# Performance work log

Hardware: AMD Instinct MI355X
Metric: run time of the kernel (lower is better)

## Reference

```python
import jax, jax.numpy as jnp
import numpy as np
import math

L, E, NH, P, MLP_H, OUT = 4, 512, 8, 16, 2048, 1024
HD = E // NH
EPS = 1e-6

def layernorm(x, g, b):
    mu = jnp.mean(x, axis=-1, keepdims=True)
    var = jnp.mean(jnp.square(x - mu), axis=-1, keepdims=True)
    return g * (x - mu) / jnp.sqrt(var + EPS) + b

def gelu_tanh(x):
    c = jnp.float32(0.7978845608028654)
    return 0.5 * x * (1.0 + jnp.tanh(c * (x + 0.044715 * x * x * x)))

def sinusoidal_pos(T, dim):
    pos = jnp.arange(T, dtype=jnp.float32)[:, None]
    div = jnp.exp(jnp.arange(0, dim, 2, dtype=jnp.float32) * (-math.log(10000.0) / dim))
    pe = jnp.concatenate([jnp.sin(pos * div), jnp.cos(pos * div)], axis=1)
    return pe[:, :dim]  # [T, dim] (all sins then all cos, matching source)

def _heads(y, B, T):
    return jnp.transpose(y.reshape(B, T, NH, HD), (0, 2, 1, 3))  # [B,H,T,D]

def self_attn(x, Wqkv, Wo):
    B, T, _ = x.shape
    q, k, v = jnp.split(x @ Wqkv, 3, axis=-1)
    q, k, v = _heads(q, B, T), _heads(k, B, T), _heads(v, B, T)
    logits = jnp.einsum('bhqd,bhkd->bhqk', q, k) * (HD ** -0.5)
    attn = jax.nn.softmax(logits, axis=-1)
    out = jnp.einsum('bhqk,bhkd->bhqd', attn, v)
    out = jnp.transpose(out, (0, 2, 1, 3)).reshape(B, T, E)
    return out @ Wo

def cross_attn(xq, xkv, Wq, Wkv, Wo):
    B, Tq, _ = xq.shape
    Tk = xkv.shape[1]
    q = _heads(xq @ Wq, B, Tq)
    k, v = jnp.split(xkv @ Wkv, 2, axis=-1)
    k, v = _heads(k, B, Tk), _heads(v, B, Tk)
    logits = jnp.einsum('bhqd,bhkd->bhqk', q, k) * (HD ** -0.5)
    attn = jax.nn.softmax(logits, axis=-1)
    out = jnp.einsum('bhqk,bhkd->bhqd', attn, v)
    out = jnp.transpose(out, (0, 2, 1, 3)).reshape(B, Tq, E)
    return out @ Wo

def block(x, i, ln1_g, ln1_b, Wqkv, Wo, ln2_g, ln2_b, W1, b1, W2, b2):
    x = x + self_attn(layernorm(x, ln1_g[i], ln1_b[i]), Wqkv[i], Wo[i])
    h = layernorm(x, ln2_g[i], ln2_b[i])
    h = gelu_tanh(h @ W1[i] + b1[i]) @ W2[i] + b2[i]
    return x + h

def setup_inputs():
    key = jax.random.key(0)
    ks = jax.random.split(key, 16)
    B, HW = 8, 512
    w = lambda k, sh: jax.random.normal(k, sh, dtype=jnp.float32) * 0.02
    return {
        'img1': jax.random.normal(ks[0], (B, HW, HW, 3), dtype=jnp.float32),
        'img2': jax.random.normal(ks[1], (B, HW, HW, 3), dtype=jnp.float32),
        'patch_W': w(ks[2], (P, P, 3, E)),
        'cls_token': w(ks[3], (1, 1, E)),
        'cls_pos': w(ks[4], (1, 1, E)),
        'ln1_g': jnp.ones((L, E)), 'ln1_b': jnp.zeros((L, E)),
        'Wqkv': w(ks[5], (L, E, 3 * E)),
        'Wo': w(ks[6], (L, E, E)),
        'ln2_g': jnp.ones((L, E)), 'ln2_b': jnp.zeros((L, E)),
        'W1': w(ks[7], (L, E, MLP_H)), 'b1': jnp.zeros((L, MLP_H)),
        'W2': w(ks[8], (L, MLP_H, E)), 'b2': jnp.zeros((L, E)),
        'Wq_c': w(ks[9], (E, E)),
        'Wkv_c': w(ks[10], (E, 2 * E)),
        'Wo_c': w(ks[11], (E, E)),
        'nf_g': jnp.ones((E,)), 'nf_b': jnp.zeros((E,)),
        'Wdec': w(ks[12], (E, OUT)), 'bdec': jnp.zeros((OUT,)),
    }

def reference(img1, img2, patch_W, cls_token, cls_pos, ln1_g, ln1_b, Wqkv, Wo,
              ln2_g, ln2_b, W1, b1, W2, b2, Wq_c, Wkv_c, Wo_c, nf_g, nf_b, Wdec, bdec):
    B = img1.shape[0]
    def embed(img):
        p = jax.lax.conv_general_dilated(img, patch_W, (P, P), 'SAME',
                                         dimension_numbers=('NHWC', 'HWIO', 'NHWC'))
        Bh, Hh, Wh, C = p.shape
        t = p.reshape(Bh, Hh * Wh, C)
        return t + sinusoidal_pos(Hh * Wh, C)[None]
    t1, t2 = embed(img1), embed(img2)
    cls = jnp.tile(cls_token + cls_pos, (B, 1, 1))
    x1 = jnp.concatenate([cls, t1], axis=1)
    x2 = jnp.concatenate([cls, t2], axis=1)
    for i in range(L):
        x1 = block(x1, i, ln1_g, ln1_b, Wqkv, Wo, ln2_g, ln2_b, W1, b1, W2, b2)
        x2 = block(x2, i, ln1_g, ln1_b, Wqkv, Wo, ln2_g, ln2_b, W1, b1, W2, b2)
    cls1, tok1 = x1[:, :1, :], x1[:, 1:, :]
    cls2, tok2 = x2[:, :1, :], x2[:, 1:, :]
    cls1 = cls1 + cross_attn(cls1, tok2, Wq_c, Wkv_c, Wo_c)
    cls2 = cls2 + cross_attn(cls2, tok1, Wq_c, Wkv_c, Wo_c)
    cls_avg = 0.5 * (cls1[:, 0, :] + cls2[:, 0, :])
    cls_avg = layernorm(cls_avg, nf_g, nf_b)
    y = cls_avg @ Wdec + bdec
    return y[:, None, None, :]  # [B,1,1,1024]
```

## Files before the change

kernel.cpp:

```cpp
#include <hip/hip_runtime.h>
#include <stdint.h>
#include <math.h>

typedef __attribute__((ext_vector_type(4))) float f4;
typedef __attribute__((ext_vector_type(8))) __bf16 bf8;
typedef __attribute__((ext_vector_type(8))) short s8;
typedef __attribute__((ext_vector_type(4))) uint32_t u32x4;

#define DI __device__ __forceinline__

DI short f2bf(float f){
  union { float f; uint32_t u; } v; v.f = f;
  uint32_t r = v.u + 0x7fffu + ((v.u >> 16) & 1u);
  return (short)(r >> 16);
}
DI float bf2f(short s){
  union { uint32_t u; float f; } v; v.u = ((uint32_t)(uint16_t)s) << 16;
  return v.f;
}
DI uint32_t cvtpk(float lo, float hi){
  uint32_t r;
  asm("v_cvt_pk_bf16_f32 %0, %1, %2" : "=v"(r) : "v"(lo), "v"(hi));
  return r;
}
DI float gelu_f(float u){
  float z = 1.5957691216057308f * u * fmaf(0.044715f, u*u, 1.f);
  return u * __builtin_amdgcn_rcpf(1.f + __expf(-z));
}
DI void gload16(const void* g, void* l){
  __builtin_amdgcn_global_load_lds((const __attribute__((address_space(1))) unsigned*)g,
                                   (__attribute__((address_space(3))) unsigned*)l, 16, 0, 0);
}

__global__ __launch_bounds__(256)
void k_transpose(const float* __restrict__ in, short* __restrict__ out, int K, int N, size_t stride)
{
  __shared__ float t[32][33];
  in  += (size_t)blockIdx.z * stride;
  out += (size_t)blockIdx.z * stride;
  int n0 = blockIdx.x*32, k0 = blockIdx.y*32;
  int tx = threadIdx.x, ty = threadIdx.y;
  #pragma unroll
  for (int i=0;i<32;i+=8) t[ty+i][tx] = in[(size_t)(k0+ty+i)*N + n0+tx];
  __syncthreads();
  #pragma unroll
  for (int i=0;i<32;i+=8) out[(size_t)(n0+ty+i)*K + k0+tx] = f2bf(t[tx][ty+i]);
}

__global__ void k_pe(float* __restrict__ pe)
{
  int p = blockIdx.x;
  for (int d = threadIdx.x; d < 512; d += 256){
    int j = (d < 256) ? d : d - 256;
    float div = expf((float)(2*j) * (-9.210340371976184f/512.f));
    float a = (float)p * div;
    pe[(size_t)p*512 + d] = (d < 256) ? sinf(a) : cosf(a);
  }
}

__global__ __launch_bounds__(256)
void k_gather(const float* __restrict__ img1, const float* __restrict__ img2, short* __restrict__ patches)
{
  int row = blockIdx.x;
  int img = row >> 13;
  int b   = (row >> 10) & 7;
  int p   = row & 1023;
  int ph = p >> 5, pw = p & 31;
  const float* src = (img ? img2 : img1) + (size_t)b*512*512*3;
  short* dst = patches + (size_t)row*768;
  for (int k = threadIdx.x; k < 768; k += 256){
    int i = k / 48; int rem = k - i*48; int j = rem / 3; int c = rem - j*3;
    int yy = ph*16 + i, xx = pw*16 + j;
    dst[k] = f2bf(src[((size_t)yy*512 + xx)*3 + c]);
  }
}

__global__ void k_zeropad(float* __restrict__ x)
{
  int idx = blockIdx.x; int ib = idx / 31; int t = 1025 + (idx - ib*31);
  x[((size_t)ib*1056 + t)*512 + threadIdx.x] = 0.f;
}
__global__ void k_cls(const float* __restrict__ ct, const float* __restrict__ cp, float* __restrict__ x)
{
  int ib = blockIdx.x; int e = threadIdx.x;
  x[(size_t)ib*1056*512 + e] = ct[e] + cp[e];
}

__global__ __launch_bounds__(256)
void k_layernorm(const float* __restrict__ x, short* __restrict__ y,
                 const float* __restrict__ g, const float* __restrict__ b)
{
  int row = blockIdx.x*4 + (threadIdx.x>>6);
  int l = threadIdx.x & 63;
  const float* xr = x + (size_t)row*512 + l*8;
  f4 v0 = *(const f4*)xr;
  f4 v1 = *(const f4*)(xr+4);
  float s = v0[0]+v0[1]+v0[2]+v0[3]+v1[0]+v1[1]+v1[2]+v1[3];
  float q = v0[0]*v0[0]+v0[1]*v0[1]+v0[2]*v0[2]+v0[3]*v0[3]
          + v1[0]*v1[0]+v1[1]*v1[1]+v1[2]*v1[2]+v1[3]*v1[3];
  #pragma unroll
  for (int m=1;m<64;m<<=1){ s += __shfl_xor(s,m); q += __shfl_xor(q,m); }
  float mu = s * 0.001953125f;
  float var = q * 0.001953125f - mu*mu;
  float rstd = rsqrtf(var + 1e-6f);
  const float* gp = g + l*8;
  const float* bp = b + l*8;
  float ov[8];
  #pragma unroll
  for (int j=0;j<8;j++){
    float xv = (j<4) ? v0[j] : v1[j-4];
    ov[j] = gp[j]*(xv-mu)*rstd + bp[j];
  }
  u32x4 pk;
  #pragma unroll
  for (int j=0;j<4;j++) pk[j] = cvtpk(ov[2*j], ov[2*j+1]);
  *(u32x4*)(y + (size_t)row*512 + l*8) = pk;
}

__global__ void k_cast_bf16(const float* __restrict__ in, short* __restrict__ out)
{
  size_t i = (size_t)blockIdx.x*256 + threadIdx.x;
  const float* p = in + i*8;
  u32x4 pk;
  #pragma unroll
  for (int j=0;j<4;j++) pk[j] = cvtpk(p[2*j], p[2*j+1]);
  *(u32x4*)(out + i*8) = pk;
}

struct EpiArgs { short* outb; float* outf; const float* bias; const float* pe; short* vT; };

template<int EPI>
__global__ __launch_bounds__(256)
void k_gemm(const short* __restrict__ A, const short* __restrict__ Bt,
            int M, int N, int K, EpiArgs ea)
{
  __shared__ short Al[128*64];
  __shared__ short Bl[128*64];
  const int tid = threadIdx.x;
  const int l = tid & 63;
  const int w = tid >> 6;
  const int wr = (w >> 1) * 64, wc = (w & 1) * 64;
  const int lr = l & 15, lg = l >> 4;
  const int brow = blockIdx.y * 128, bcol = blockIdx.x * 128;
  const short* Ab = A  + (size_t)brow * K;
  const short* Bb = Bt + (size_t)bcol * K;
  f4 acc[4][4];
  #pragma unroll
  for (int m=0;m<4;m++)
    #pragma unroll
    for (int n=0;n<4;n++){ acc[m][n][0]=0.f; acc[m][n][1]=0.f; acc[m][n][2]=0.f; acc[m][n][3]=0.f; }

  const int rsw = lr & 7;
  for (int kt = 0; kt < K; kt += 64){
    #pragma unroll
    for (int i=0;i<4;i++){
      int s   = i*256 + tid;
      int row = s >> 3;
      int gs  = (s & 7) ^ (row & 7);
      gload16(Ab + (size_t)row*K + kt + gs*8, &Al[s*8]);
      gload16(Bb + (size_t)row*K + kt + gs*8, &Bl[s*8]);
    }
    __syncthreads();
    #pragma unroll
    for (int ko=0;ko<2;ko++){
      bf8 af[4], bfr[4];
      const int ps = ((ko*4 + lg) ^ rsw) * 8;
      #pragma unroll
      for (int m=0;m<4;m++) af[m]  = *(const bf8*)&Al[(wr + m*16 + lr)*64 + ps];
      #pragma unroll
      for (int n=0;n<4;n++) bfr[n] = *(const bf8*)&Bl[(wc + n*16 + lr)*64 + ps];
      #pragma unroll
      for (int m=0;m<4;m++)
        #pragma unroll
        for (int n=0;n<4;n++)
          acc[m][n] = __builtin_amdgcn_mfma_f32_16x16x32_bf16(af[m], bfr[n], acc[m][n], 0, 0, 0);
    }
    __syncthreads();
  }

  #pragma unroll
  for (int m=0;m<4;m++){
    #pragma unroll
    for (int n=0;n<4;n++){
      const int row0 = brow + wr + m*16 + lg*4;
      const int col  = bcol + wc + n*16 + lr;
      float v0 = acc[m][n][0], v1 = acc[m][n][1], v2 = acc[m][n][2], v3 = acc[m][n][3];
      if (EPI == 0 || EPI == 1){
        if (EPI == 1 && col < 512){ v0*=0.125f; v1*=0.125f; v2*=0.125f; v3*=0.125f; }
        uint32_t u01 = cvtpk(v0, v1), u23 = cvtpk(v2, v3);
        short s0 = (short)u01, s1 = (short)(u01>>16), s2 = (short)u23, s3 = (short)(u23>>16);
        ea.outb[(size_t)(row0+0)*N + col] = s0;
        ea.outb[(size_t)(row0+1)*N + col] = s1;
        ea.outb[(size_t)(row0+2)*N + col] = s2;
        ea.outb[(size_t)(row0+3)*N + col] = s3;
        if (EPI == 1 && col >= 1024){
          int ib = row0 / 1056, t = row0 - ib*1056;
          short* vtb = ea.vT + ((size_t)ib*512 + (col - 1024))*1056;
          vtb[t] = s0; vtb[t+1] = s1; vtb[t+2] = s2; vtb[t+3] = s3;
        }
      } else if (EPI == 2){
        float bv = ea.bias ? ea.bias[col] : 0.f;
        ea.outf[(size_t)(row0+0)*N + col] += v0 + bv;
        ea.outf[(size_t)(row0+1)*N + col] += v1 + bv;
        ea.outf[(size_t)(row0+2)*N + col] += v2 + bv;
        ea.outf[(size_t)(row0+3)*N + col] += v3 + bv;
      } else if (EPI == 3){
        float bv = ea.bias[col];
        float g0 = gelu_f(v0+bv), g1 = gelu_f(v1+bv), g2 = gelu_f(v2+bv), g3 = gelu_f(v3+bv);
        uint32_t u01 = cvtpk(g0, g1), u23 = cvtpk(g2, g3);
        ea.outb[(size_t)(row0+0)*N + col] = (short)u01;
        ea.outb[(size_t)(row0+1)*N + col] = (short)(u01>>16);
        ea.outb[(size_t)(row0+2)*N + col] = (short)u23;
        ea.outb[(size_t)(row0+3)*N + col] = (short)(u23>>16);
      } else if (EPI == 4){
        #pragma unroll
        for (int r=0;r<4;r++){
          int row = row0 + r;
          int ib = row >> 10, p = row & 1023;
          float v = (r==0)?v0:(r==1)?v1:(r==2)?v2:v3;
          ea.outf[((size_t)(ib*1056 + 1 + p))*512 + col] = v + ea.pe[(size_t)p*512 + col];
        }
      }
    }
  }
}

__global__ __launch_bounds__(256)
void k_attn(const short* __restrict__ qkv, const short* __restrict__ vT, short* __restrict__ aout)
{
  __shared__ short Pl[4][2][32*40];
  __shared__ float Sc[4][2][32];

  const int w  = threadIdx.x >> 6;
  const int qt = blockIdx.x * 4 + w;
  if (qt > 32) return;
  const int u  = blockIdx.y;
  const int ib = u >> 3, h = u & 7;
  const int l = threadIdx.x & 63, lr = l & 15, lg = l >> 4;
  const size_t rb = (size_t)ib * 1056;
  const int t0 = qt * 32;

  bf8 qf[2][2];
  #pragma unroll
  for (int nq=0;nq<2;nq++)
    #pragma unroll
    for (int ks=0;ks<2;ks++)
      qf[nq][ks] = *(const bf8*)&qkv[(rb + t0 + nq*16 + lr)*1536 + h*64 + ks*32 + lg*8];

  f4 o[2][4];
  float mrun[2], lrun[2];
  #pragma unroll
  for (int mq=0;mq<2;mq++)
    #pragma unroll
    for (int nd=0;nd<4;nd++){ o[mq][nd][0]=0.f; o[mq][nd][1]=0.f; o[mq][nd][2]=0.f; o[mq][nd][3]=0.f; }
  mrun[0]=mrun[1]=-1e30f; lrun[0]=lrun[1]=0.f;

  auto tile = [&](int jt, bool MASK){
    const int j0 = jt*32;
    const int pb = jt & 1;
    bf8 kf[2][2];
    #pragma unroll
    for (int mk=0;mk<2;mk++)
      #pragma unroll
      for (int ks=0;ks<2;ks++)
        kf[mk][ks] = *(const bf8*)&qkv[(rb + j0 + mk*16 + lr)*1536 + 512 + h*64 + ks*32 + lg*8];
    bf8 vb[4];
    #pragma unroll
    for (int nd=0;nd<4;nd++)
      vb[nd] = *(const bf8*)&vT[((size_t)ib*512 + h*64 + nd*16 + lr)*1056 + j0 + lg*8];

    f4 st[2][2];
    #pragma unroll
    for (int mk=0;mk<2;mk++)
      #pragma unroll
      for (int nq=0;nq<2;nq++){ st[mk][nq][0]=0.f; st[mk][nq][1]=0.f; st[mk][nq][2]=0.f; st[mk][nq][3]=0.f; }
    #pragma unroll
    for (int ks=0;ks<2;ks++)
      #pragma unroll
      for (int mk=0;mk<2;mk++)
        #pragma unroll
        for (int nq=0;nq<2;nq++)
          st[mk][nq] = __builtin_amdgcn_mfma_f32_16x16x32_bf16(kf[mk][ks], qf[nq][ks], st[mk][nq], 0, 0, 0);

    float p8[2][8], mx[2];
    #pragma unroll
    for (int nq=0;nq<2;nq++){
      mx[nq] = -1e30f;
      #pragma unroll
      for (int mk=0;mk<2;mk++)
        #pragma unroll
        for (int r=0;r<4;r++){
          float v = st[mk][nq][r];
          if (MASK){
            int kk = j0 + mk*16 + lg*4 + r;
            v = (kk > 1024) ? -1e30f : v;
          }
          p8[nq][mk*4+r] = v;
          mx[nq] = fmaxf(mx[nq], v);
        }
      mx[nq] = fmaxf(mx[nq], __shfl_xor(mx[nq], 16));
      mx[nq] = fmaxf(mx[nq], __shfl_xor(mx[nq], 32));
    }

    bool ok = (mx[0] <= mrun[0] + 8.f) && (mx[1] <= mrun[1] + 8.f);
    if (__all(ok)){
      #pragma unroll
      for (int nq=0;nq<2;nq++){
        float rs = 0.f;
        #pragma unroll
        for (int i=0;i<8;i++){ float p = __expf(p8[nq][i] - mrun[nq]); p8[nq][i] = p; rs += p; }
        rs += __shfl_xor(rs, 16);
        rs += __shfl_xor(rs, 32);
        lrun[nq] += rs;
        uint32_t* prow = (uint32_t*)&Pl[w][pb][(nq*16 + lr)*40];
        #pragma unroll
        for (int mk=0;mk<2;mk++){
          prow[mk*8 + lg*2]     = cvtpk(p8[nq][mk*4+0], p8[nq][mk*4+1]);
          prow[mk*8 + lg*2 + 1] = cvtpk(p8[nq][mk*4+2], p8[nq][mk*4+3]);
        }
      }
      asm volatile("s_waitcnt lgkmcnt(0)" ::: "memory");
      __builtin_amdgcn_sched_barrier(0);
      bf8 pa[2];
      #pragma unroll
      for (int mq=0;mq<2;mq++) pa[mq] = *(const bf8*)&Pl[w][pb][(mq*16 + lr)*40 + lg*8];
      #pragma unroll
      for (int mq=0;mq<2;mq++)
        #pragma unroll
        for (int nd=0;nd<4;nd++)
          o[mq][nd] = __builtin_amdgcn_mfma_f32_16x16x32_bf16(pa[mq], vb[nd], o[mq][nd], 0, 0, 0);
    } else {
      #pragma unroll
      for (int nq=0;nq<2;nq++){
        float mn = fmaxf(mrun[nq], mx[nq]);
        float sc = __expf(mrun[nq] - mn);
        mrun[nq] = mn;
        float rs = 0.f;
        #pragma unroll
        for (int i=0;i<8;i++){ float p = __expf(p8[nq][i] - mn); p8[nq][i] = p; rs += p; }
        rs += __shfl_xor(rs, 16);
        rs += __shfl_xor(rs, 32);
        lrun[nq] = lrun[nq]*sc + rs;
        Sc[w][pb][nq*16 + lr] = sc;
        uint32_t* prow = (uint32_t*)&Pl[w][pb][(nq*16 + lr)*40];
        #pragma unroll
        for (int mk=0;mk<2;mk++){
          prow[mk*8 + lg*2]     = cvtpk(p8[nq][mk*4+0], p8[nq][mk*4+1]);
          prow[mk*8 + lg*2 + 1] = cvtpk(p8[nq][mk*4+2], p8[nq][mk*4+3]);
        }
      }
      asm volatile("s_waitcnt lgkmcnt(0)" ::: "memory");
      __builtin_amdgcn_sched_barrier(0);
      f4 scv[2]; bf8 pa[2];
      #pragma unroll
      for (int mq=0;mq<2;mq++){
        scv[mq] = *(const f4*)&Sc[w][pb][mq*16 + lg*4];
        pa[mq]  = *(const bf8*)&Pl[w][pb][(mq*16 + lr)*40 + lg*8];
      }
      #pragma unroll
      for (int mq=0;mq<2;mq++)
        #pragma unroll
        for (int nd=0;nd<4;nd++){
          #pragma unroll
          for (int r=0;r<4;r++) o[mq][nd][r] *= scv[mq][r];
        }
      #pragma unroll
      for (int mq=0;mq<2;mq++)
        #pragma unroll
        for (int nd=0;nd<4;nd++)
          o[mq][nd] = __builtin_amdgcn_mfma_f32_16x16x32_bf16(pa[mq], vb[nd], o[mq][nd], 0, 0, 0);
    }
  };

  for (int jt=0; jt<32; jt++) tile(jt, false);
  tile(32, true);

  #pragma unroll
  for (int nq=0;nq<2;nq++) Sc[w][1][nq*16 + lr] = lrun[nq];
  asm volatile("s_waitcnt lgkmcnt(0)" ::: "memory");
  __builtin_amdgcn_sched_barrier(0);
  #pragma unroll
  for (int mq=0;mq<2;mq++){
    f4 lsv = *(const f4*)&Sc[w][1][mq*16 + lg*4];
    float i0 = __builtin_amdgcn_rcpf(lsv[0]);
    float i1 = __builtin_amdgcn_rcpf(lsv[1]);
    float i2 = __builtin_amdgcn_rcpf(lsv[2]);
    float i3 = __builtin_amdgcn_rcpf(lsv[3]);
    const size_t base = rb + t0 + mq*16 + lg*4;
    #pragma unroll
    for (int nd=0;nd<4;nd++){
      int col = h*64 + nd*16 + lr;
      uint32_t u01 = cvtpk(o[mq][nd][0]*i0, o[mq][nd][1]*i1);
      uint32_t u23 = cvtpk(o[mq][nd][2]*i2, o[mq][nd][3]*i3);
      aout[(base+0)*512 + col] = (short)u01;
      aout[(base+1)*512 + col] = (short)(u01>>16);
      aout[(base+2)*512 + col] = (short)u23;
      aout[(base+3)*512 + col] = (short)(u23>>16);
    }
  }
}

__global__ __launch_bounds__(256)
void k_cross_q(const float* __restrict__ x, const float* __restrict__ Wq, float* __restrict__ qc)
{
  __shared__ float xs[512];
  int ib = blockIdx.x;
  const float* xr = x + (size_t)ib*1056*512;
  for (int e=threadIdx.x;e<512;e+=256) xs[e] = xr[e];
  __syncthreads();
  for (int n=threadIdx.x;n<512;n+=256){
    float acc = 0.f;
    for (int k=0;k<512;k++) acc += xs[k]*Wq[(size_t)k*512 + n];
    qc[(size_t)ib*512 + n] = acc;
  }
}

__global__ __launch_bounds__(64)
void k_cross_attn(const float* __restrict__ qc, const short* __restrict__ kv, float* __restrict__ oc)
{
  int u = blockIdx.x; int ib = u >> 3, h = u & 7;
  int img = ib >> 3, b = ib & 7;
  int sib = (1 - img)*8 + b;
  int l = threadIdx.x;
  __shared__ float qs[64];
  __shared__ float pl[1024];
  qs[l] = qc[(size_t)ib*512 + h*64 + l];
  __syncthreads();
  float lmax = -1e30f;
  for (int jj=0; jj<16; jj++){
    int j = jj*64 + l;
    const short* kr = kv + ((size_t)(sib*1056 + 1 + j))*1024 + h*64;
    float acc = 0.f;
    for (int d=0; d<64; d++) acc += qs[d]*bf2f(kr[d]);
    acc *= 0.125f;
    pl[j] = acc;
    lmax = fmaxf(lmax, acc);
  }
  #pragma unroll
  for (int m=1;m<64;m<<=1) lmax = fmaxf(lmax, __shfl_xor(lmax, m));
  __syncthreads();
  float lsum = 0.f;
  for (int jj=0; jj<16; jj++){
    int j = jj*64 + l;
    float p = __expf(pl[j] - lmax);
    pl[j] = p; lsum += p;
  }
  #pragma unroll
  for (int m=1;m<64;m<<=1) lsum += __shfl_xor(lsum, m);
  __syncthreads();
  float acc = 0.f;
  for (int j=0;j<1024;j++)
    acc += pl[j] * bf2f(kv[((size_t)(sib*1056 + 1 + j))*1024 + 512 + h*64 + l]);
  oc[(size_t)ib*512 + h*64 + l] = acc / lsum;
}

__global__ __launch_bounds__(256)
void k_cross_out(const float* __restrict__ x, const float* __restrict__ oc,
                 const float* __restrict__ Wo, float* __restrict__ cn)
{
  __shared__ float os[512];
  int ib = blockIdx.x;
  for (int e=threadIdx.x;e<512;e+=256) os[e] = oc[(size_t)ib*512+e];
  __syncthreads();
  for (int n=threadIdx.x;n<512;n+=256){
    float acc = 0.f;
    for (int k=0;k<512;k++) acc += os[k]*Wo[(size_t)k*512+n];
    cn[(size_t)ib*512+n] = x[(size_t)ib*1056*512 + n] + acc;
  }
}

__global__ __launch_bounds__(256)
void k_final(const float* __restrict__ cn, const float* __restrict__ nfg, const float* __restrict__ nfb,
             const float* __restrict__ Wdec, const float* __restrict__ bdec, float* __restrict__ out)
{
  int b = blockIdx.x;
  __shared__ float a[512];
  __shared__ float an[512];
  __shared__ float red[8];
  int tid = threadIdx.x;
  float s = 0.f, q = 0.f;
  for (int e=tid;e<512;e+=256){
    float av = 0.5f*(cn[(size_t)b*512 + e] + cn[(size_t)(8+b)*512 + e]);
    a[e] = av; s += av; q += av*av;
  }
  #pragma unroll
  for (int m=1;m<64;m<<=1){ s += __shfl_xor(s,m); q += __shfl_xor(q,m); }
  int w = tid>>6;
  if ((tid&63)==0){ red[w] = s; red[4+w] = q; }
  __syncthreads();
  s = red[0]+red[1]+red[2]+red[3];
  q = red[4]+red[5]+red[6]+red[7];
  float mu = s*0.001953125f;
  float var = q*0.001953125f - mu*mu;
  float rstd = rsqrtf(var + 1e-6f);
  for (int e=tid;e<512;e+=256) an[e] = nfg[e]*(a[e]-mu)*rstd + nfb[e];
  __syncthreads();
  for (int n=tid;n<1024;n+=256){
    float acc = bdec[n];
    for (int e=0;e<512;e++) acc += an[e]*Wdec[(size_t)e*1024 + n];
    out[(size_t)b*1024 + n] = acc;
  }
}

extern "C" void kernel_launch(void* const* d_in, const int* in_sizes, int n_in,
                              void* d_out, int out_size, void* d_ws, size_t ws_size,
                              hipStream_t stream)
{
  (void)in_sizes; (void)n_in;
  const float* img1 = (const float*)d_in[0];
  const float* img2 = (const float*)d_in[1];
  const float* patchW = (const float*)d_in[2];
  const float* cls_t = (const float*)d_in[3];
  const float* cls_p = (const float*)d_in[4];
  const float* ln1g = (const float*)d_in[5];
  const float* ln1b = (const float*)d_in[6];
  const float* Wqkv = (const float*)d_in[7];
  const float* Wo   = (const float*)d_in[8];
  const float* ln2g = (const float*)d_in[9];
  const float* ln2b = (const float*)d_in[10];
  const float* W1   = (const float*)d_in[11];
  const float* b1   = (const float*)d_in[12];
  const float* W2   = (const float*)d_in[13];
  const float* b2   = (const float*)d_in[14];
  const float* Wqc  = (const float*)d_in[15];
  const float* Wkvc = (const float*)d_in[16];
  const float* Woc  = (const float*)d_in[17];
  const float* nfg  = (const float*)d_in[18];
  const float* nfb  = (const float*)d_in[19];
  const float* Wdec = (const float*)d_in[20];
  const float* bdec = (const float*)d_in[21];
  float* out = (float*)d_out;

  const size_t offA = 34603008, offB = 51904512, offC = 121110528, offD = 148111360;
  const size_t NEEDED = 148209664;
  if (ws_size < NEEDED){
    hipMemsetAsync(d_out, 0, (size_t)out_size*sizeof(float), stream);
    return;
  }
  char* ws = (char*)d_ws;
  float* x    = (float*)ws;
  short* y    = (short*)(ws + offA);
  short* attn = y;
  short* qkv  = (short*)(ws + offB);
  short* vT   = (short*)(ws + offB + 51904512);
  short* mh   = (short*)(ws + offB);
  short* patches = (short*)(ws + offB);
  float* pe   = (float*)(ws + offB + 25165824);
  short* kvc  = (short*)(ws + offB);
  short* wts  = (short*)(ws + offC);
  float* qc   = (float*)(ws + offD);
  float* oc   = (float*)(ws + offD + 32768);
  float* cn   = (float*)(ws + offD + 65536);

  short* patchWt = wts;
  short* WqkvT = wts + 393216;
  short* WoT   = wts + 3538944;
  short* W1T   = wts + 4587520;
  short* W2T   = wts + 8781824;
  short* WkvT  = wts + 12976128;

  dim3 tb(32,8,1);
  k_transpose<<<dim3(16,24,1), tb, 0, stream>>>(patchW, patchWt, 768, 512, (size_t)768*512);
  k_transpose<<<dim3(48,16,4), tb, 0, stream>>>(Wqkv, WqkvT, 512, 1536, (size_t)512*1536);
  k_transpose<<<dim3(16,16,4), tb, 0, stream>>>(Wo,   WoT,   512, 512,  (size_t)512*512);
  k_transpose<<<dim3(64,16,4), tb, 0, stream>>>(W1,   W1T,   512, 2048, (size_t)512*2048);
  k_transpose<<<dim3(16,64,4), tb, 0, stream>>>(W2,   W2T,   2048, 512, (size_t)2048*512);
  k_transpose<<<dim3(32,16,1), tb, 0, stream>>>(Wkvc, WkvT,  512, 1024, (size_t)512*1024);

  k_pe<<<1024, 256, 0, stream>>>(pe);
  k_gather<<<16384, 256, 0, stream>>>(img1, img2, patches);
  k_zeropad<<<496, 512, 0, stream>>>(x);
  k_cls<<<16, 512, 0, stream>>>(cls_t, cls_p, x);

  EpiArgs ea;
  ea = EpiArgs{nullptr, x, nullptr, pe, nullptr};
  k_gemm<4><<<dim3(4, 128), 256, 0, stream>>>(patches, patchWt, 16384, 512, 768, ea);

  for (int i=0;i<4;i++){
    k_layernorm<<<4224, 256, 0, stream>>>(x, y, ln1g + i*512, ln1b + i*512);
    ea = EpiArgs{qkv, nullptr, nullptr, nullptr, vT};
    k_gemm<1><<<dim3(12, 132), 256, 0, stream>>>(y, WqkvT + (size_t)i*1536*512, 16896, 1536, 512, ea);
    k_attn<<<dim3(9, 128), 256, 0, stream>>>(qkv, vT, attn);
    ea = EpiArgs{nullptr, x, nullptr, nullptr, nullptr};
    k_gemm<2><<<dim3(4, 132), 256, 0, stream>>>(attn, WoT + (size_t)i*512*512, 16896, 512, 512, ea);
    k_layernorm<<<4224, 256, 0, stream>>>(x, y, ln2g + i*512, ln2b + i*512);
    ea = EpiArgs{mh, nullptr, b1 + i*2048, nullptr, nullptr};
    k_gemm<3><<<dim3(16, 132), 256, 0, stream>>>(y, W1T + (size_t)i*2048*512, 16896, 2048, 512, ea);
    ea = EpiArgs{nullptr, x, b2 + i*512, nullptr, nullptr};
    k_gemm<2><<<dim3(4, 132), 256, 0, stream>>>(mh, W2T + (size_t)i*512*2048, 16896, 512, 2048, ea);
  }

  k_cast_bf16<<<4224, 256, 0, stream>>>(x, y);
  ea = EpiArgs{kvc, nullptr, nullptr, nullptr, nullptr};
  k_gemm<0><<<dim3(8, 132), 256, 0, stream>>>(y, WkvT, 16896, 1024, 512, ea);
  k_cross_q<<<16, 256, 0, stream>>>(x, Wqc, qc);
  k_cross_attn<<<128, 64, 0, stream>>>(qc, kvc, oc);
  k_cross_out<<<16, 256, 0, stream>>>(x, oc, Woc, cn);
  k_final<<<8, 256, 0, stream>>>(cn, nfg, nfb, Wdec, bdec, out);
}
```

Measured before the change: 1.751 ms.

## Prefetch next K tile in attention loop and raise priority around MFMAs

The self-attention kernel now double-buffers K fragments in registers, issuing the loads for tile j+1 while tile j's QK^T and PV MFMAs run, with the loop unrolled by two to swap buffers. It also brackets the MFMA groups with s_setprio so waves in the matrix phase get issue priority over waves in softmax. The aim is to hide global-load latency for K behind compute. The cost is higher register pressure from the second K buffer, which could lower occupancy. This is only one kernel within the larger pipeline.

```diff
diff --git a/kernel.cpp b/kernel.cpp
--- a/kernel.cpp
+++ b/kernel.cpp
@@ -247,6 +247,9 @@
     for (int ks=0;ks<2;ks++)
       qf[nq][ks] = *(const bf8*)&qkv[(rb + t0 + nq*16 + lr)*1536 + h*64 + ks*32 + lg*8];
 
+  const short* kbase = &qkv[(rb + lr)*1536 + 512 + h*64 + lg*8];
+  const short* vbase = &vT[((size_t)ib*512 + h*64 + lr)*1056 + lg*8];
+
   f4 o[2][4];
   float mrun[2], lrun[2];
   #pragma unroll
@@ -255,32 +258,38 @@
     for (int nd=0;nd<4;nd++){ o[mq][nd][0]=0.f; o[mq][nd][1]=0.f; o[mq][nd][2]=0.f; o[mq][nd][3]=0.f; }
   mrun[0]=mrun[1]=-1e30f; lrun[0]=lrun[1]=0.f;
 
-  auto tile = [&](int jt, bool MASK){
+  auto LD_K = [&](bf8 (&kf)[2][2], int jt){
+    const short* kb = kbase + (size_t)jt*32*1536;
+    #pragma unroll
+    for (int mk=0;mk<2;mk++)
+      #pragma unroll
+      for (int ks=0;ks<2;ks++)
+        kf[mk][ks] = *(const bf8*)(kb + (size_t)mk*16*1536 + ks*32);
+  };
+
+  auto TILE = [&](int jt, bf8 (&kc)[2][2], bf8 (&kn)[2][2], bool MASK){
     const int j0 = jt*32;
     const int pb = jt & 1;
-    bf8 kf[2][2];
+    bf8 vb[4];
+    #pragma unroll
+    for (int nd=0;nd<4;nd++)
+      vb[nd] = *(const bf8*)(vbase + (size_t)nd*16*1056 + j0);
+    if (!MASK) LD_K(kn, jt+1);
+
+    f4 st[2][2];
     #pragma unroll
     for (int mk=0;mk<2;mk++)
       #pragma unroll
-      for (int ks=0;ks<2;ks++)
-        kf[mk][ks] = *(const bf8*)&qkv[(rb + j0 + mk*16 + lr)*1536 + 512 + h*64 + ks*32 + lg*8];
-    bf8 vb[4];
-    #pragma unroll
-    for (int nd=0;nd<4;nd++)
-      vb[nd] = *(const bf8*)&vT[((size_t)ib*512 + h*64 + nd*16 + lr)*1056 + j0 + lg*8];
-
-    f4 st[2][2];
-    #pragma unroll
-    for (int mk=0;mk<2;mk++)
-      #pragma unroll
       for (int nq=0;nq<2;nq++){ st[mk][nq][0]=0.f; st[mk][nq][1]=0.f; st[mk][nq][2]=0.f; st[mk][nq][3]=0.f; }
+    __builtin_amdgcn_s_setprio(1);
     #pragma unroll
     for (int ks=0;ks<2;ks++)
       #pragma unroll
       for (int mk=0;mk<2;mk++)
         #pragma unroll
         for (int nq=0;nq<2;nq++)
-          st[mk][nq] = __builtin_amdgcn_mfma_f32_16x16x32_bf16(kf[mk][ks], qf[nq][ks], st[mk][nq], 0, 0, 0);
+          st[mk][nq] = __builtin_amdgcn_mfma_f32_16x16x32_bf16(kc[mk][ks], qf[nq][ks], st[mk][nq], 0, 0, 0);
+    __builtin_amdgcn_s_setprio(0);
 
     float p8[2][8], mx[2];
     #pragma unroll
@@ -324,11 +333,13 @@
       bf8 pa[2];
       #pragma unroll
       for (int mq=0;mq<2;mq++) pa[mq] = *(const bf8*)&Pl[w][pb][(mq*16 + lr)*40 + lg*8];
+      __builtin_amdgcn_s_setprio(1);
       #pragma unroll
       for (int mq=0;mq<2;mq++)
         #pragma unroll
         for (int nd=0;nd<4;nd++)
           o[mq][nd] = __builtin_amdgcn_mfma_f32_16x16x32_bf16(pa[mq], vb[nd], o[mq][nd], 0, 0, 0);
+      __builtin_amdgcn_s_setprio(0);
     } else {
       #pragma unroll
       for (int nq=0;nq<2;nq++){
@@ -364,16 +375,24 @@
           #pragma unroll
           for (int r=0;r<4;r++) o[mq][nd][r] *= scv[mq][r];
         }
+      __builtin_amdgcn_s_setprio(1);
       #pragma unroll
       for (int mq=0;mq<2;mq++)
         #pragma unroll
         for (int nd=0;nd<4;nd++)
           o[mq][nd] = __builtin_amdgcn_mfma_f32_16x16x32_bf16(pa[mq], vb[nd], o[mq][nd], 0, 0, 0);
+      __builtin_amdgcn_s_setprio(0);
     }
   };
 
-  for (int jt=0; jt<32; jt++) tile(jt, false);
-  tile(32, true);
+  bf8 kA[2][2], kB[2][2];
+  LD_K(kA, 0);
+  #pragma unroll 1
+  for (int j2=0; j2<16; j2++){
+    TILE(2*j2,   kA, kB, false);
+    TILE(2*j2+1, kB, kA, false);
+  }
+  TILE(32, kA, kB, true);
 
   #pragma unroll
   for (int nq=0;nq<2;nq++) Sc[w][1][nq*16 + lr] = lrun[nq];
```

Measured after the change: 1.694 ms. -3.3%, faster.

## Stage K/V tiles through swizzled shared memory with double buffering in attention

Applied to the files above, without the earlier changes.

The attention kernel now loads each 32-key K and V tile once per block into XOR-swizzled LDS buffers using direct global-to-LDS loads. Previously each of the four waves fetched its own copy from global memory. The next tile's load is issued before the current tile's compute, so the copies are double-buffered, and the MFMA sections run at raised wave priority. Waves past the last query tile stay alive to take part in the block barriers and skip only the final store. The cost is one __syncthreads per tile and some idle waves in the last block.

```diff
diff --git a/kernel.cpp b/kernel.cpp
--- a/kernel.cpp
+++ b/kernel.cpp
@@ -228,15 +228,18 @@
 __global__ __launch_bounds__(256)
 void k_attn(const short* __restrict__ qkv, const short* __restrict__ vT, short* __restrict__ aout)
 {
+  __shared__ __align__(16) short Kl[2][32*64];
+  __shared__ __align__(16) short Vl[2][64*32];
   __shared__ short Pl[4][2][32*40];
   __shared__ float Sc[4][2][32];
 
-  const int w  = threadIdx.x >> 6;
-  const int qt = blockIdx.x * 4 + w;
-  if (qt > 32) return;
+  const int tid = threadIdx.x;
+  const int w  = tid >> 6;
+  const int qtR = blockIdx.x * 4 + w;
+  const int qt  = qtR > 32 ? 32 : qtR;
   const int u  = blockIdx.y;
   const int ib = u >> 3, h = u & 7;
-  const int l = threadIdx.x & 63, lr = l & 15, lg = l >> 4;
+  const int l = tid & 63, lr = l & 15, lg = l >> 4;
   const size_t rb = (size_t)ib * 1056;
   const int t0 = qt * 32;
 
@@ -255,32 +258,55 @@
     for (int nd=0;nd<4;nd++){ o[mq][nd][0]=0.f; o[mq][nd][1]=0.f; o[mq][nd][2]=0.f; o[mq][nd][3]=0.f; }
   mrun[0]=mrun[1]=-1e30f; lrun[0]=lrun[1]=0.f;
 
-  auto tile = [&](int jt, bool MASK){
+  auto STAGE = [&](int buf, int jt){
     const int j0 = jt*32;
-    const int pb = jt & 1;
-    bf8 kf[2][2];
+    {
+      int krow = tid >> 3, ks = tid & 7;
+      int gs = ks ^ (krow & 7);
+      gload16(&qkv[(rb + j0 + krow)*1536 + 512 + h*64 + gs*8], &Kl[buf][tid*8]);
+    }
+    {
+      int vrow = tid >> 2, vs = tid & 3;
+      int gs = vs ^ (vrow & 3);
+      gload16(&vT[((size_t)ib*512 + h*64 + vrow)*1056 + j0 + gs*8], &Vl[buf][tid*8]);
+    }
+  };
+
+  STAGE(0, 0);
+
+  for (int jt=0; jt<=32; jt++){
+    const int cur = jt & 1;
+    const int pb  = cur;
+    const bool MASK = (jt == 32);
+    const int j0 = jt*32;
+    __syncthreads();
+
+    bf8 kc[2][2], vb[4];
     #pragma unroll
     for (int mk=0;mk<2;mk++)
       #pragma unroll
       for (int ks=0;ks<2;ks++)
-        kf[mk][ks] = *(const bf8*)&qkv[(rb + j0 + mk*16 + lr)*1536 + 512 + h*64 + ks*32 + lg*8];
-    bf8 vb[4];
+        kc[mk][ks] = *(const bf8*)&Kl[cur][((mk*16+lr)*8 + ((ks*4+lg) ^ (lr&7)))*8];
     #pragma unroll
     for (int nd=0;nd<4;nd++)
-      vb[nd] = *(const bf8*)&vT[((size_t)ib*512 + h*64 + nd*16 + lr)*1056 + j0 + lg*8];
+      vb[nd] = *(const bf8*)&Vl[cur][((nd*16+lr)*4 + (lg ^ (lr&3)))*8];
+
+    if (jt < 32) STAGE(cur^1, jt+1);
 
     f4 st[2][2];
     #pragma unroll
     for (int mk=0;mk<2;mk++)
       #pragma unroll
       for (int nq=0;nq<2;nq++){ st[mk][nq][0]=0.f; st[mk][nq][1]=0.f; st[mk][nq][2]=0.f; st[mk][nq][3]=0.f; }
+    __builtin_amdgcn_s_setprio(1);
     #pragma unroll
     for (int ks=0;ks<2;ks++)
       #pragma unroll
       for (int mk=0;mk<2;mk++)
         #pragma unroll
         for (int nq=0;nq<2;nq++)
-          st[mk][nq] = __builtin_amdgcn_mfma_f32_16x16x32_bf16(kf[mk][ks], qf[nq][ks], st[mk][nq], 0, 0, 0);
+          st[mk][nq] = __builtin_amdgcn_mfma_f32_16x16x32_bf16(kc[mk][ks], qf[nq][ks], st[mk][nq], 0, 0, 0);
+    __builtin_amdgcn_s_setprio(0);
 
     float p8[2][8], mx[2];
     #pragma unroll
@@ -324,11 +350,13 @@
       bf8 pa[2];
       #pragma unroll
       for (int mq=0;mq<2;mq++) pa[mq] = *(const bf8*)&Pl[w][pb][(mq*16 + lr)*40 + lg*8];
+      __builtin_amdgcn_s_setprio(1);
       #pragma unroll
       for (int mq=0;mq<2;mq++)
         #pragma unroll
         for (int nd=0;nd<4;nd++)
           o[mq][nd] = __builtin_amdgcn_mfma_f32_16x16x32_bf16(pa[mq], vb[nd], o[mq][nd], 0, 0, 0);
+      __builtin_amdgcn_s_setprio(0);
     } else {
       #pragma unroll
       for (int nq=0;nq<2;nq++){
@@ -364,38 +392,39 @@
           #pragma unroll
           for (int r=0;r<4;r++) o[mq][nd][r] *= scv[mq][r];
         }
+      __builtin_amdgcn_s_setprio(1);
       #pragma unroll
       for (int mq=0;mq<2;mq++)
         #pragma unroll
         for (int nd=0;nd<4;nd++)
           o[mq][nd] = __builtin_amdgcn_mfma_f32_16x16x32_bf16(pa[mq], vb[nd], o[mq][nd], 0, 0, 0);
-    }
-  };
-
-  for (int jt=0; jt<32; jt++) tile(jt, false);
-  tile(32, true);
-
-  #pragma unroll
-  for (int nq=0;nq<2;nq++) Sc[w][1][nq*16 + lr] = lrun[nq];
-  asm volatile("s_waitcnt lgkmcnt(0)" ::: "memory");
-  __builtin_amdgcn_sched_barrier(0);
-  #pragma unroll
-  for (int mq=0;mq<2;mq++){
-    f4 lsv = *(const f4*)&Sc[w][1][mq*16 + lg*4];
-    float i0 = __builtin_amdgcn_rcpf(lsv[0]);
-    float i1 = __builtin_amdgcn_rcpf(lsv[1]);
-    float i2 = __builtin_amdgcn_rcpf(lsv[2]);
-    float i3 = __builtin_amdgcn_rcpf(lsv[3]);
-    const size_t base = rb + t0 + mq*16 + lg*4;
-    #pragma unroll
-    for (int nd=0;nd<4;nd++){
-      int col = h*64 + nd*16 + lr;
-      uint32_t u01 = cvtpk(o[mq][nd][0]*i0, o[mq][nd][1]*i1);
-      uint32_t u23 = cvtpk(o[mq][nd][2]*i2, o[mq][nd][3]*i3);
-      aout[(base+0)*512 + col] = (short)u01;
-      aout[(base+1)*512 + col] = (short)(u01>>16);
-      aout[(base+2)*512 + col] = (short)u23;
-      aout[(base+3)*512 + col] = (short)(u23>>16);
+      __builtin_amdgcn_s_setprio(0);
+    }
+  }
+
+  if (qtR <= 32){
+    #pragma unroll
+    for (int nq=0;nq<2;nq++) Sc[w][1][nq*16 + lr] = lrun[nq];
+    asm volatile("s_waitcnt lgkmcnt(0)" ::: "memory");
+    __builtin_amdgcn_sched_barrier(0);
+    #pragma unroll
+    for (int mq=0;mq<2;mq++){
+      f4 lsv = *(const f4*)&Sc[w][1][mq*16 + lg*4];
+      float i0 = __builtin_amdgcn_rcpf(lsv[0]);
+      float i1 = __builtin_amdgcn_rcpf(lsv[1]);
+      float i2 = __builtin_amdgcn_rcpf(lsv[2]);
+      float i3 = __builtin_amdgcn_rcpf(lsv[3]);
+      const size_t base = rb + t0 + mq*16 + lg*4;
+      #pragma unroll
+      for (int nd=0;nd<4;nd++){
+        int col = h*64 + nd*16 + lr;
+        uint32_t u01 = cvtpk(o[mq][nd][0]*i0, o[mq][nd][1]*i1);
+        uint32_t u23 = cvtpk(o[mq][nd][2]*i2, o[mq][nd][3]*i3);
+        aout[(base+0)*512 + col] = (short)u01;
+        aout[(base+1)*512 + col] = (short)(u01>>16);
+        aout[(base+2)*512 + col] = (short)u23;
+        aout[(base+3)*512 + col] = (short)(u23>>16);
+      }
     }
   }
 }
```

Measured after the change: 1.623 ms. 1.08x faster.
